# Performance work log

Hardware: AMD Instinct MI355X
Metric: run time of the kernel (lower is better)

The kernel has to match this reference:

```python
import jax, jax.numpy as jnp
import numpy as np

HEADS = 8
DIM_HEAD = 32
SCALE = DIM_HEAD ** -0.5


def _split_heads(t):
    # [b, n, h*d] -> [b, h, n, d]
    b, n, hd = t.shape
    return t.reshape(b, n, HEADS, hd // HEADS).transpose(0, 2, 1, 3)


def setup_inputs() -> dict:
    key = jax.random.key(0)
    k1, k2, k3, k4 = jax.random.split(key, 4)
    b, n, dim = 2, 2048, 256
    inner = HEADS * DIM_HEAD  # 256
    x = jax.random.normal(k1, (b, n, dim), dtype=jnp.float32)
    attn_feat = jax.random.normal(k2, (b, n, dim), dtype=jnp.float32)
    # nn.Linear(dim, 3*inner, bias=False): store as [dim, 3*inner] for x @ W
    W_qkv = jax.random.normal(k3, (dim, 3 * inner), dtype=jnp.float32) * (dim ** -0.5)
    W_qkv_aux = jax.random.normal(k4, (dim, 3 * inner), dtype=jnp.float32) * (dim ** -0.5)
    return {"x": x, "attn_feat": attn_feat, "W_qkv": W_qkv, "W_qkv_aux": W_qkv_aux,
            "use_cls_tokens": 1}


def reference(x, attn_feat, W_qkv, W_qkv_aux, use_cls_tokens):
    b, n, dim = x.shape
    # aux Q,K (v_aux computed but unused, matching original chunk of 3)
    qkv_aux = attn_feat @ W_qkv_aux            # [b, n, 3*inner]
    q_aux, k_aux, _ = jnp.split(qkv_aux, 3, axis=-1)
    q_aux, k_aux = _split_heads(q_aux), _split_heads(k_aux)
    # self Q,K
    qkv_self = x @ W_qkv
    q_self, k_self, _ = jnp.split(qkv_self, 3, axis=-1)
    q_self, k_self = _split_heads(q_self), _split_heads(k_self)
    # dual score product: (QK^T_aux * scale) * (QK^T_self * scale)
    dots_aux = jnp.einsum('bhid,bhjd->bhij', q_aux, k_aux) * SCALE
    dots_self = jnp.einsum('bhid,bhjd->bhij', q_self, k_self) * SCALE
    attn = jax.nn.softmax(dots_aux * dots_self, axis=-1)  # [b, h, n, n]
    # v = x.unsqueeze(1): broadcast raw x over heads
    out = jnp.einsum('bhij,bjd->bhid', attn, x)           # [b, h, n, dim]
    out = out.transpose(0, 2, 1, 3).reshape(b, n, HEADS * dim)
    attn_flat = attn.transpose(0, 2, 1, 3).reshape(b, n, HEADS * n)
    return (out, out[:, 0], attn_flat[:, 0])
```

## Files before the change

### kernel.cpp

```cpp
#include <hip/hip_runtime.h>

typedef _Float16 f16;
typedef _Float16 f16x4 __attribute__((ext_vector_type(4)));
typedef _Float16 f16x8 __attribute__((ext_vector_type(8)));
typedef float f32x4 __attribute__((ext_vector_type(4)));

#define LOG2E 1.4426950408889634f
#define SCL   (1.4426950408889634f / 32.0f)
#define TH_RAW 177.445f

__global__ __launch_bounds__(256) void k_transpose(const float* __restrict__ x,
                                                   f16* __restrict__ xt) {
  __shared__ f16 tile[64][65];
  int n0 = blockIdx.x * 64;
  int d0 = blockIdx.y * 64;
  int b  = blockIdx.z;
  int t = threadIdx.x;
  int colr = t & 63, rowg = t >> 6;
#pragma unroll
  for (int r = 0; r < 16; ++r) {
    int row = r * 4 + rowg;
    tile[row][colr] = (f16)x[((size_t)b * 2048 + n0 + row) * 256 + d0 + colr];
  }
  __syncthreads();
#pragma unroll
  for (int r = 0; r < 16; ++r) {
    int drow = r * 4 + rowg;
    xt[((size_t)b * 256 + d0 + drow) * 2048 + n0 + colr] = tile[colr][drow];
  }
}

__global__ __launch_bounds__(256) void k_transW(const float* __restrict__ Wq,
    const float* __restrict__ Wa, f16* __restrict__ Wt) {
  __shared__ f16 tile[64][65];
  int n0 = blockIdx.x * 64, k0 = blockIdx.y * 64, s = blockIdx.z;
  const float* W = s ? Wa : Wq;
  f16* dst = Wt + (size_t)s * 512 * 256;
  int t = threadIdx.x, c = t & 63, rg = t >> 6;
#pragma unroll
  for (int r = 0; r < 16; ++r) {
    int krow = r * 4 + rg;
    tile[krow][c] = (f16)W[(size_t)(k0 + krow) * 768 + n0 + c];
  }
  __syncthreads();
#pragma unroll
  for (int r = 0; r < 16; ++r) {
    int nrow = r * 4 + rg;
    dst[(size_t)(n0 + nrow) * 256 + k0 + c] = tile[c][nrow];
  }
}

__global__ __launch_bounds__(256) void k_proj(const float* __restrict__ x,
    const float* __restrict__ af, const f16* __restrict__ Wt,
    f16* __restrict__ Qs, f16* __restrict__ Ks,
    f16* __restrict__ Qa, f16* __restrict__ Ka) {
  int mt = blockIdx.x, nt = blockIdx.y, s = blockIdx.z;
  const float* A = s ? af : x;
  const f16* W = Wt + (size_t)s * 512 * 256;
  f16* Qd = s ? Qa : Qs;
  f16* Kd = s ? Ka : Ks;
  int t = threadIdx.x, wv = t >> 6, ln = t & 63, cl = ln & 15, g = ln >> 4;
  int m0 = mt * 64, n0 = nt * 64;
  const float* arow = A + (size_t)(m0 + wv * 16 + cl) * 256 + g * 8;
  const f16* wb = W + (size_t)n0 * 256 + g * 8;
  f32x4 z4 = {0.f, 0.f, 0.f, 0.f};
  f32x4 acc[4] = {z4, z4, z4, z4};
#pragma unroll
  for (int k32 = 0; k32 < 8; ++k32) {
    float4 u = *(const float4*)(arow + k32 * 32);
    float4 v = *(const float4*)(arow + k32 * 32 + 4);
    f16x8 a = { (f16)u.x, (f16)u.y, (f16)u.z, (f16)u.w,
                (f16)v.x, (f16)v.y, (f16)v.z, (f16)v.w };
#pragma unroll
    for (int n4 = 0; n4 < 4; ++n4) {
      f16x8 bf = *(const f16x8*)(wb + (size_t)(n4 * 16 + cl) * 256 + k32 * 32);
      acc[n4] = __builtin_amdgcn_mfma_f32_16x16x32_f16(a, bf, acc[n4], 0, 0, 0);
    }
  }
#pragma unroll
  for (int n4 = 0; n4 < 4; ++n4) {
    int c = n0 + n4 * 16 + cl;
    int head = (c & 255) >> 5, d = c & 31;
    f16* dst = (c < 256) ? Qd : Kd;
#pragma unroll
    for (int r = 0; r < 4; ++r) {
      int m = m0 + wv * 16 + g * 4 + r;
      int bb = m >> 11, nn = m & 2047;
      dst[(((size_t)bb * 8 + head) * 2048 + nn) * 32 + d] = (f16)acc[n4][r];
    }
  }
}

__global__ __launch_bounds__(256, 2) void k_flash(const f16* __restrict__ Qs,
    const f16* __restrict__ Ks, const f16* __restrict__ Qa,
    const f16* __restrict__ Ka, const f16* __restrict__ xt,
    float* __restrict__ out, float* __restrict__ out_cls) {
  __shared__ f16 PL[2][64][72];
  __shared__ float alphaL[2][64] __attribute__((aligned(16)));
  __shared__ int   rsF[2][4] __attribute__((aligned(16)));
  __shared__ float lL[64];
  int qt = blockIdx.x, h = blockIdx.y, b = blockIdx.z;
  int bh = b * 8 + h;
  int t = threadIdx.x, wv = t >> 6, ln = t & 63, cl = ln & 15, g = ln >> 4;
  int qrow0 = qt * 64 + wv * 16;
  f16x8 qsf = *(const f16x8*)&Qs[((size_t)bh * 2048 + qrow0 + cl) * 32 + g * 8];
  f16x8 qaf = *(const f16x8*)&Qa[((size_t)bh * 2048 + qrow0 + cl) * 32 + g * 8];
  f32x4 z4 = {0.f, 0.f, 0.f, 0.f};
  f32x4 acc[4][4];
#pragma unroll
  for (int i = 0; i < 4; ++i)
#pragma unroll
    for (int j = 0; j < 4; ++j) acc[i][j] = z4;
  float m_run = -3.0e38f, l_lane = 0.f;
  const f16* kaBase = Ka + ((size_t)bh * 2048 + cl) * 32 + g * 8;
  const f16* ksBase = Ks + ((size_t)bh * 2048 + cl) * 32 + g * 8;
  const f16* xb = xt + ((size_t)b * 256 + wv * 64) * 2048;

  float tv[16];
  f16x8 xf[2][4];
  f16x8 kaA[4], ksA[4], kaB[4], ksB[4];

  auto LOADK = [&](int kt, f16x8 (&ka)[4], f16x8 (&ks)[4]) {
#pragma unroll
    for (int jt = 0; jt < 4; ++jt) {
      ka[jt] = *(const f16x8*)(kaBase + (size_t)(kt * 64 + jt * 16) * 32);
      ks[jt] = *(const f16x8*)(ksBase + (size_t)(kt * 64 + jt * 16) * 32);
    }
  };

  auto SCORE_MM = [&](f16x8 (&ka)[4], f16x8 (&ks)[4]) {
#pragma unroll
    for (int jt = 0; jt < 4; ++jt) {
      f32x4 za = __builtin_amdgcn_mfma_f32_16x16x32_f16(ka[jt], qaf, z4, 0, 0, 0);
      f32x4 zs = __builtin_amdgcn_mfma_f32_16x16x32_f16(ks[jt], qsf, z4, 0, 0, 0);
#pragma unroll
      for (int r = 0; r < 4; ++r) tv[jt * 4 + r] = za[r] * zs[r];
    }
  };

  auto SCORE_FIN = [&](int buf) {
    float a0 = fmaxf(tv[0], tv[1]),   a1 = fmaxf(tv[2], tv[3]);
    float a2 = fmaxf(tv[4], tv[5]),   a3 = fmaxf(tv[6], tv[7]);
    float a4 = fmaxf(tv[8], tv[9]),   a5 = fmaxf(tv[10], tv[11]);
    float a6 = fmaxf(tv[12], tv[13]), a7 = fmaxf(tv[14], tv[15]);
    float b0 = fmaxf(a0, a1), b1 = fmaxf(a2, a3);
    float b2 = fmaxf(a4, a5), b3 = fmaxf(a6, a7);
    float lmax = fmaxf(fmaxf(b0, b1), fmaxf(b2, b3));
    int wflag = 0;
    if (__any(lmax > m_run + TH_RAW)) {
      float tm = fmaxf(lmax, __shfl_xor(lmax, 16, 64));
      tm = fmaxf(tm, __shfl_xor(tm, 32, 64));
      float m_new = fmaxf(m_run, tm);
      float alpha = exp2f((m_run - m_new) * SCL);
      l_lane *= alpha;
      m_run = m_new;
      if (g == 0) alphaL[buf][wv * 16 + cl] = alpha;
      wflag = 1;
    }
    float mS = m_run * SCL;
    float p[16];
#pragma unroll
    for (int i = 0; i < 16; ++i) p[i] = exp2f(fmaf(tv[i], SCL, -mS));
    float s0 = p[0] + p[1],   s1 = p[2] + p[3];
    float s2 = p[4] + p[5],   s3 = p[6] + p[7];
    float s4 = p[8] + p[9],   s5 = p[10] + p[11];
    float s6 = p[12] + p[13], s7 = p[14] + p[15];
    float u0 = s0 + s1, u1 = s2 + s3, u2 = s4 + s5, u3 = s6 + s7;
    l_lane += (u0 + u1) + (u2 + u3);
#pragma unroll
    for (int jt = 0; jt < 4; ++jt) {
      auto lo = __builtin_amdgcn_cvt_pkrtz(p[jt * 4 + 0], p[jt * 4 + 1]);
      auto hi = __builtin_amdgcn_cvt_pkrtz(p[jt * 4 + 2], p[jt * 4 + 3]);
      f16x4 pk = { (f16)lo[0], (f16)lo[1], (f16)hi[0], (f16)hi[1] };
      *(f16x4*)&PL[buf][wv * 16 + cl][jt * 16 + g * 4] = pk;
    }
    if (ln == 0) rsF[buf][wv] = wflag;
  };

  auto XFLOAD = [&](int kt) {
#pragma unroll
    for (int ks2 = 0; ks2 < 2; ++ks2)
#pragma unroll
      for (int ddt = 0; ddt < 4; ++ddt)
        xf[ks2][ddt] = *(const f16x8*)(xb + (size_t)(ddt * 16 + cl) * 2048 +
                                       kt * 64 + ks2 * 32 + g * 8);
  };

  auto PVDO = [&](int pbuf) {
    int4 fl = *(const int4*)&rsF[pbuf][0];
    int flq[4] = { fl.x, fl.y, fl.z, fl.w };
#pragma unroll
    for (int qt2 = 0; qt2 < 4; ++qt2) {
      if (flq[qt2]) {
        f32x4 a4 = *(const f32x4*)&alphaL[pbuf][qt2 * 16 + g * 4];
#pragma unroll
        for (int ddt = 0; ddt < 4; ++ddt)
#pragma unroll
          for (int r = 0; r < 4; ++r) acc[qt2][ddt][r] *= a4[r];
      }
    }
#pragma unroll
    for (int ks2 = 0; ks2 < 2; ++ks2) {
      f16x8 pf[4];
#pragma unroll
      for (int qt2 = 0; qt2 < 4; ++qt2)
        pf[qt2] = *(const f16x8*)&PL[pbuf][qt2 * 16 + cl][ks2 * 32 + g * 8];
#pragma unroll
      for (int ddt = 0; ddt < 4; ++ddt)
#pragma unroll
        for (int qt2 = 0; qt2 < 4; ++qt2)
          acc[qt2][ddt] = __builtin_amdgcn_mfma_f32_16x16x32_f16(
              pf[qt2], xf[ks2][ddt], acc[qt2][ddt], 0, 0, 0);
    }
  };

  LOADK(0, kaA, ksA);
  LOADK(1, kaB, ksB);
  SCORE_MM(kaA, ksA);
  SCORE_FIN(0);
  __syncthreads();

  for (int k2 = 0; k2 < 15; ++k2) {
    int k = 2 * k2 + 1;
    XFLOAD(k - 1);
    LOADK(k + 1, kaA, ksA);
    SCORE_MM(kaB, ksB);
    PVDO(0);
    SCORE_FIN(1);
    __syncthreads();
    XFLOAD(k);
    LOADK(k + 2, kaB, ksB);
    SCORE_MM(kaA, ksA);
    PVDO(1);
    SCORE_FIN(0);
    __syncthreads();
  }

  XFLOAD(30);
  SCORE_MM(kaB, ksB);
  PVDO(0);
  SCORE_FIN(1);
  __syncthreads();
  XFLOAD(31);
  PVDO(1);

  l_lane += __shfl_xor(l_lane, 16, 64);
  l_lane += __shfl_xor(l_lane, 32, 64);
  if (g == 0) lL[wv * 16 + cl] = l_lane;
  __syncthreads();
#pragma unroll
  for (int qt2 = 0; qt2 < 4; ++qt2) {
#pragma unroll
    for (int r = 0; r < 4; ++r) {
      float linv = 1.0f / lL[qt2 * 16 + g * 4 + r];
      int q = qt * 64 + qt2 * 16 + g * 4 + r;
#pragma unroll
      for (int ddt = 0; ddt < 4; ++ddt) {
        float v = acc[qt2][ddt][r] * linv;
        int col = h * 256 + wv * 64 + ddt * 16 + cl;
        out[((size_t)b * 2048 + q) * 2048 + col] = v;
        if (q == 0) out_cls[(size_t)b * 2048 + col] = v;
      }
    }
  }
}

__global__ __launch_bounds__(256) void k_attn0(const f16* __restrict__ Qs,
    const f16* __restrict__ Ks, const f16* __restrict__ Qa,
    const f16* __restrict__ Ka, float* __restrict__ dst) {
  __shared__ float qa_s[32], qs_s[32];
  __shared__ float red[256];
  int h = blockIdx.x, b = blockIdx.y, bh = b * 8 + h;
  int t = threadIdx.x;
  if (t < 32) {
    qa_s[t] = (float)Qa[(size_t)bh * 2048 * 32 + t];
    qs_s[t] = (float)Qs[(size_t)bh * 2048 * 32 + t];
  }
  __syncthreads();
  float sv[8];
#pragma unroll
  for (int r = 0; r < 8; ++r) {
    int j = r * 256 + t;
    const f16x8* ka8 = (const f16x8*)&Ka[((size_t)bh * 2048 + j) * 32];
    const f16x8* ks8 = (const f16x8*)&Ks[((size_t)bh * 2048 + j) * 32];
    float da = 0.f, ds = 0.f;
#pragma unroll
    for (int c = 0; c < 4; ++c) {
      f16x8 va = ka8[c], vs = ks8[c];
#pragma unroll
      for (int d = 0; d < 8; ++d) {
        da += qa_s[c * 8 + d] * (float)va[d];
        ds += qs_s[c * 8 + d] * (float)vs[d];
      }
    }
    sv[r] = da * ds * (1.f / 32.f);
  }
  float mx = sv[0];
#pragma unroll
  for (int r = 1; r < 8; ++r) mx = fmaxf(mx, sv[r]);
  red[t] = mx;
  __syncthreads();
  for (int st = 128; st > 0; st >>= 1) {
    if (t < st) red[t] = fmaxf(red[t], red[t + st]);
    __syncthreads();
  }
  float m = red[0];
  __syncthreads();
  float e[8], sum = 0.f;
#pragma unroll
  for (int r = 0; r < 8; ++r) {
    e[r] = exp2f((sv[r] - m) * LOG2E);
    sum += e[r];
  }
  red[t] = sum;
  __syncthreads();
  for (int st = 128; st > 0; st >>= 1) {
    if (t < st) red[t] += red[t + st];
    __syncthreads();
  }
  float l = red[0];
#pragma unroll
  for (int r = 0; r < 8; ++r)
    dst[(size_t)b * 16384 + h * 2048 + r * 256 + t] = e[r] / l;
}

extern "C" void kernel_launch(void* const* d_in, const int* in_sizes, int n_in,
                              void* d_out, int out_size, void* d_ws, size_t ws_size,
                              hipStream_t stream) {
  const float* x  = (const float*)d_in[0];
  const float* af = (const float*)d_in[1];
  const float* Wq = (const float*)d_in[2];
  const float* Wa = (const float*)d_in[3];
  const size_t QK = (size_t)2 * 8 * 2048 * 32;
  f16* Qs = (f16*)d_ws;
  f16* Ks = Qs + QK;
  f16* Qa = Ks + QK;
  f16* Ka = Qa + QK;
  f16* xt = Ka + QK;
  f16* Wt = xt + QK;
  float* out     = (float*)d_out;
  float* out_cls = out + (size_t)2 * 2048 * 2048;
  float* attn0   = out_cls + 2 * 2048;

  k_transpose<<<dim3(32, 4, 2), 256, 0, stream>>>(x, xt);
  k_transW<<<dim3(8, 4, 2), 256, 0, stream>>>(Wq, Wa, Wt);
  k_proj<<<dim3(64, 8, 2), 256, 0, stream>>>(x, af, Wt, Qs, Ks, Qa, Ka);
  k_flash<<<dim3(32, 8, 2), 256, 0, stream>>>(Qs, Ks, Qa, Ka, xt, out, out_cls);
  k_attn0<<<dim3(8, 2), 256, 0, stream>>>(Qs, Ks, Qa, Ka, attn0);
}
```

Before: 211.8 us.

## Specialize flash kernel warps into score producers and PV consumers

Doubles the block to 512 threads and splits waves by role. Four waves compute the dual QK scores and softmax, and the other four run the P·V MFMAs one tile behind, handing off through a double-buffered LDS P tile. K tiles for both Q/K pairs are now staged cooperatively in LDS instead of each wave loading them into registers. This is meant to overlap the score/exp work with the PV matrix multiply and cut register pressure per wave. The costs are an extra barrier per tile, more LDS traffic, and a launch bound of 4 blocks per CU that may force register spilling.

```diff
diff --git a/kernel.cpp b/kernel.cpp
--- a/kernel.cpp
+++ b/kernel.cpp
@@ -91,10 +91,12 @@
   }
 }
 
-__global__ __launch_bounds__(256, 2) void k_flash(const f16* __restrict__ Qs,
+__global__ __launch_bounds__(512, 4) void k_flash(const f16* __restrict__ Qs,
     const f16* __restrict__ Ks, const f16* __restrict__ Qa,
     const f16* __restrict__ Ka, const f16* __restrict__ xt,
     float* __restrict__ out, float* __restrict__ out_cls) {
+  __shared__ f16 KaL[2][64][40];
+  __shared__ f16 KsL[2][64][40];
   __shared__ f16 PL[2][64][72];
   __shared__ float alphaL[2][64] __attribute__((aligned(16)));
   __shared__ int   rsF[2][4] __attribute__((aligned(16)));
@@ -102,37 +104,39 @@
   int qt = blockIdx.x, h = blockIdx.y, b = blockIdx.z;
   int bh = b * 8 + h;
   int t = threadIdx.x, wv = t >> 6, ln = t & 63, cl = ln & 15, g = ln >> 4;
-  int qrow0 = qt * 64 + wv * 16;
-  f16x8 qsf = *(const f16x8*)&Qs[((size_t)bh * 2048 + qrow0 + cl) * 32 + g * 8];
-  f16x8 qaf = *(const f16x8*)&Qa[((size_t)bh * 2048 + qrow0 + cl) * 32 + g * 8];
+  bool isScore = wv < 4;
+  int sw = wv & 3;
   f32x4 z4 = {0.f, 0.f, 0.f, 0.f};
+
+  int sel = t >> 8;
+  int krow = (t >> 2) & 63, koff = (t & 3) * 8;
+  f16 (*KLsel)[64][40] = sel ? KsL : KaL;
+  const f16* kSrc = (sel ? Ks : Ka) + ((size_t)bh * 2048 + krow) * 32 + koff;
+
+  f16x8 qsf, qaf;
+  float m_run = -3.0e38f, l_lane = 0.f;
+  if (isScore) {
+    int qrow0 = qt * 64 + sw * 16;
+    qsf = *(const f16x8*)&Qs[((size_t)bh * 2048 + qrow0 + cl) * 32 + g * 8];
+    qaf = *(const f16x8*)&Qa[((size_t)bh * 2048 + qrow0 + cl) * 32 + g * 8];
+  }
+  float tv[16];
+
   f32x4 acc[4][4];
 #pragma unroll
   for (int i = 0; i < 4; ++i)
 #pragma unroll
     for (int j = 0; j < 4; ++j) acc[i][j] = z4;
-  float m_run = -3.0e38f, l_lane = 0.f;
-  const f16* kaBase = Ka + ((size_t)bh * 2048 + cl) * 32 + g * 8;
-  const f16* ksBase = Ks + ((size_t)bh * 2048 + cl) * 32 + g * 8;
-  const f16* xb = xt + ((size_t)b * 256 + wv * 64) * 2048;
-
-  float tv[16];
+  const f16* xb = xt + ((size_t)b * 256 + sw * 64) * 2048;
   f16x8 xf[2][4];
-  f16x8 kaA[4], ksA[4], kaB[4], ksB[4];
-
-  auto LOADK = [&](int kt, f16x8 (&ka)[4], f16x8 (&ks)[4]) {
+
+  auto SCORE_MM = [&](int buf) {
 #pragma unroll
     for (int jt = 0; jt < 4; ++jt) {
-      ka[jt] = *(const f16x8*)(kaBase + (size_t)(kt * 64 + jt * 16) * 32);
-      ks[jt] = *(const f16x8*)(ksBase + (size_t)(kt * 64 + jt * 16) * 32);
-    }
-  };
-
-  auto SCORE_MM = [&](f16x8 (&ka)[4], f16x8 (&ks)[4]) {
-#pragma unroll
-    for (int jt = 0; jt < 4; ++jt) {
-      f32x4 za = __builtin_amdgcn_mfma_f32_16x16x32_f16(ka[jt], qaf, z4, 0, 0, 0);
-      f32x4 zs = __builtin_amdgcn_mfma_f32_16x16x32_f16(ks[jt], qsf, z4, 0, 0, 0);
+      f16x8 kaf = *(const f16x8*)&KaL[buf][jt * 16 + cl][g * 8];
+      f16x8 ksf = *(const f16x8*)&KsL[buf][jt * 16 + cl][g * 8];
+      f32x4 za = __builtin_amdgcn_mfma_f32_16x16x32_f16(kaf, qaf, z4, 0, 0, 0);
+      f32x4 zs = __builtin_amdgcn_mfma_f32_16x16x32_f16(ksf, qsf, z4, 0, 0, 0);
 #pragma unroll
       for (int r = 0; r < 4; ++r) tv[jt * 4 + r] = za[r] * zs[r];
     }
@@ -154,7 +158,7 @@
       float alpha = exp2f((m_run - m_new) * SCL);
       l_lane *= alpha;
       m_run = m_new;
-      if (g == 0) alphaL[buf][wv * 16 + cl] = alpha;
+      if (g == 0) alphaL[buf][sw * 16 + cl] = alpha;
       wflag = 1;
     }
     float mS = m_run * SCL;
@@ -172,9 +176,9 @@
       auto lo = __builtin_amdgcn_cvt_pkrtz(p[jt * 4 + 0], p[jt * 4 + 1]);
       auto hi = __builtin_amdgcn_cvt_pkrtz(p[jt * 4 + 2], p[jt * 4 + 3]);
       f16x4 pk = { (f16)lo[0], (f16)lo[1], (f16)hi[0], (f16)hi[1] };
-      *(f16x4*)&PL[buf][wv * 16 + cl][jt * 16 + g * 4] = pk;
-    }
-    if (ln == 0) rsF[buf][wv] = wflag;
+      *(f16x4*)&PL[buf][sw * 16 + cl][jt * 16 + g * 4] = pk;
+    }
+    if (ln == 0) rsF[buf][sw] = wflag;
   };
 
   auto XFLOAD = [&](int kt) {
@@ -214,52 +218,48 @@
     }
   };
 
-  LOADK(0, kaA, ksA);
-  LOADK(1, kaB, ksB);
-  SCORE_MM(kaA, ksA);
-  SCORE_FIN(0);
-  __syncthreads();
-
-  for (int k2 = 0; k2 < 15; ++k2) {
-    int k = 2 * k2 + 1;
-    XFLOAD(k - 1);
-    LOADK(k + 1, kaA, ksA);
-    SCORE_MM(kaB, ksB);
-    PVDO(0);
-    SCORE_FIN(1);
+  *(f16x8*)&KLsel[0][krow][koff] = *(const f16x8*)kSrc;
+  __syncthreads();
+
+  for (int k = 0; k < 32; ++k) {
+    int buf = k & 1;
+    f16x8 kreg;
+    if (k < 31) kreg = *(const f16x8*)(kSrc + (size_t)(k + 1) * 2048);
+    if (isScore) {
+      SCORE_MM(buf);
+      SCORE_FIN(buf);
+    } else if (k > 0) {
+      XFLOAD(k - 1);
+      PVDO(buf ^ 1);
+    }
+    if (k < 31) *(f16x8*)&KLsel[buf ^ 1][krow][koff] = kreg;
     __syncthreads();
-    XFLOAD(k);
-    LOADK(k + 2, kaB, ksB);
-    SCORE_MM(kaA, ksA);
+  }
+
+  if (isScore) {
+    l_lane += __shfl_xor(l_lane, 16, 64);
+    l_lane += __shfl_xor(l_lane, 32, 64);
+    if (g == 0) lL[sw * 16 + cl] = l_lane;
+  } else {
+    XFLOAD(31);
     PVDO(1);
-    SCORE_FIN(0);
-    __syncthreads();
-  }
-
-  XFLOAD(30);
-  SCORE_MM(kaB, ksB);
-  PVDO(0);
-  SCORE_FIN(1);
-  __syncthreads();
-  XFLOAD(31);
-  PVDO(1);
-
-  l_lane += __shfl_xor(l_lane, 16, 64);
-  l_lane += __shfl_xor(l_lane, 32, 64);
-  if (g == 0) lL[wv * 16 + cl] = l_lane;
-  __syncthreads();
-#pragma unroll
-  for (int qt2 = 0; qt2 < 4; ++qt2) {
-#pragma unroll
-    for (int r = 0; r < 4; ++r) {
-      float linv = 1.0f / lL[qt2 * 16 + g * 4 + r];
-      int q = qt * 64 + qt2 * 16 + g * 4 + r;
-#pragma unroll
-      for (int ddt = 0; ddt < 4; ++ddt) {
-        float v = acc[qt2][ddt][r] * linv;
-        int col = h * 256 + wv * 64 + ddt * 16 + cl;
-        out[((size_t)b * 2048 + q) * 2048 + col] = v;
-        if (q == 0) out_cls[(size_t)b * 2048 + col] = v;
+  }
+  __syncthreads();
+
+  if (!isScore) {
+#pragma unroll
+    for (int qt2 = 0; qt2 < 4; ++qt2) {
+#pragma unroll
+      for (int r = 0; r < 4; ++r) {
+        float linv = 1.0f / lL[qt2 * 16 + g * 4 + r];
+        int q = qt * 64 + qt2 * 16 + g * 4 + r;
+#pragma unroll
+        for (int ddt = 0; ddt < 4; ++ddt) {
+          float v = acc[qt2][ddt][r] * linv;
+          int col = h * 256 + sw * 64 + ddt * 16 + cl;
+          out[((size_t)b * 2048 + q) * 2048 + col] = v;
+          if (q == 0) out_cls[(size_t)b * 2048 + col] = v;
+        }
       }
     }
   }
@@ -345,6 +345,6 @@
   k_transpose<<<dim3(32, 4, 2), 256, 0, stream>>>(x, xt);
   k_transW<<<dim3(8, 4, 2), 256, 0, stream>>>(Wq, Wa, Wt);
   k_proj<<<dim3(64, 8, 2), 256, 0, stream>>>(x, af, Wt, Qs, Ks, Qa, Ka);
-  k_flash<<<dim3(32, 8, 2), 256, 0, stream>>>(Qs, Ks, Qa, Ka, xt, out, out_cls);
+  k_flash<<<dim3(32, 8, 2), 512, 0, stream>>>(Qs, Ks, Qa, Ka, xt, out, out_cls);
   k_attn0<<<dim3(8, 2), 256, 0, stream>>>(Qs, Ks, Qa, Ka, attn0);
 }
```

Measured after the change: 244.4 us. 1.15x slower.
